# Kernel tuning notes

Hardware: AMD Instinct MI355X
Metric: run time of the kernel (lower is better)

## Reference

```python
import jax, jax.numpy as jnp
import numpy as np

B, S, H, I, E, K = 2, 512, 768, 3072, 8, 1
LB_COEF = 0.01


def _xavier(key, shape, fan_in, fan_out):
    limit = np.sqrt(6.0 / (fan_in + fan_out)).astype(np.float32)
    return jax.random.uniform(key, shape, jnp.float32, -limit, limit)


def setup_inputs() -> dict:
    key = jax.random.key(0)
    k0, k1, k2, k3 = jax.random.split(key, 4)
    return {
        "hidden_states": jax.random.normal(k0, (B, S, H), jnp.float32),
        "gate_w": _xavier(k1, (E, H), H, E),          # nn.Linear(H, E).weight
        "gate_b": jnp.zeros((E,), jnp.float32),
        "w1": _xavier(k2, (E, I, H), H, I),           # per-expert Linear(H, I).weight
        "b1": jnp.zeros((E, I), jnp.float32),
        "w2": _xavier(k3, (E, H, I), I, H),           # per-expert Linear(I, H).weight
        "b2": jnp.zeros((E, H), jnp.float32),
    }


def reference(hidden_states, gate_w, gate_b, w1, b1, w2, b2):
    b, s, h = hidden_states.shape
    x = hidden_states.reshape(-1, h)                      # [T, H]
    gate_logits = x @ gate_w.T + gate_b                   # [T, E]
    top_vals, top_idx = jax.lax.top_k(gate_logits, K)     # [T, K]
    # softmax over the (single) selected logit in fp32 -> all ones, kept for fidelity
    gate_weights = jax.nn.softmax(top_vals.astype(jnp.float32), axis=-1)  # [T, K]

    # load balancing loss (torch.var is unbiased, ddof=1)
    gate_mean = gate_logits.mean(axis=0)                  # [E]
    gate_var = gate_logits.var(axis=0, ddof=1)            # [E]
    lb_loss = LB_COEF * (gate_var / (gate_mean ** 2 + 1e-8)).mean()

    # dense per-expert FFN (exact math; combine picks the routed expert)
    hmid = jnp.einsum('th,eih->tei', x, w1) + b1          # [T, E, I]
    hmid = jax.nn.gelu(hmid, approximate=False)           # torch nn.GELU (erf)
    y = jnp.einsum('tei,ehi->teh', hmid, w2) + b2         # [T, E, H]

    sel = top_idx[:, 0]                                   # [T]
    y_sel = jnp.take_along_axis(y, sel[:, None, None], axis=1)[:, 0]  # [T, H]
    out = y_sel * gate_weights[:, 0:1]                    # weight == 1.0 for k=1
    return out.reshape(b, s, h), lb_loss
```

## Files before the change

kernel.cpp:

```cpp
#include <hip/hip_runtime.h>
#include <hip/hip_bf16.h>
#include <math.h>

#define Hdim 768
#define Idim 3072
#define Tn   1024
#define En   8
#define CAP  256
#define LD2  136

using v4f     = __attribute__((ext_vector_type(4))) float;
using short8  = __attribute__((ext_vector_type(8))) short;
using short4v = __attribute__((ext_vector_type(4))) short;

__device__ inline unsigned short f2bf(float f) {
    unsigned u = __float_as_uint(f);
    u += 0x7fffu + ((u >> 16) & 1u);
    return (unsigned short)(u >> 16);
}
__device__ inline short4v pack4(float4 v) {
    return short4v{ (short)f2bf(v.x), (short)f2bf(v.y), (short)f2bf(v.z), (short)f2bf(v.w) };
}
__device__ __forceinline__ void gl2lds16(const unsigned short* g, unsigned short* l) {
    __builtin_amdgcn_global_load_lds(
        (const __attribute__((address_space(1))) void*)g,
        (__attribute__((address_space(3))) void*)l, 16, 0, 0);
}

__global__ __launch_bounds__(256) void gate_kernel(
    const float* __restrict__ x, const float* __restrict__ gw, const float* __restrict__ gb,
    float* __restrict__ psum, float* __restrict__ psumsq,
    int* __restrict__ sel, int* __restrict__ gcur)
{
    __shared__ float gws[8 * 772];
    __shared__ float lg[8][8];
    int tid = threadIdx.x;
    long t0 = (long)blockIdx.x * 8;
    if (blockIdx.x == 0 && tid < En) gcur[tid] = 0;
    for (int i = tid; i < 8 * 768; i += 256) gws[(i / 768) * 772 + (i % 768)] = gw[i];
    __syncthreads();

    int tok = tid >> 5, e = (tid >> 2) & 7, qr = tid & 3;
    const float4* xp = (const float4*)(x + (t0 + tok) * Hdim) + qr * 48;
    const float4* gp = (const float4*)(gws + e * 772) + qr * 48;
    float a0 = 0.f, a1 = 0.f;
#pragma unroll 8
    for (int i = 0; i < 48; i += 2) {
        float4 xa = xp[i], ga = gp[i], xc = xp[i + 1], gc = gp[i + 1];
        a0 += xa.x * ga.x + xa.y * ga.y + xa.z * ga.z + xa.w * ga.w;
        a1 += xc.x * gc.x + xc.y * gc.y + xc.z * gc.z + xc.w * gc.w;
    }
    float acc = a0 + a1;
    acc += __shfl_xor(acc, 1);
    acc += __shfl_xor(acc, 2);
    if (qr == 0) lg[tok][e] = acc + gb[e];
    __syncthreads();

    if (tid < 8) {
        float best = lg[tid][0]; int bi = 0;
        for (int j = 1; j < 8; j++) { float v = lg[tid][j]; if (v > best) { best = v; bi = j; } }
        sel[t0 + tid] = bi;
    } else if (tid < 16) {
        int e2 = tid - 8;
        float s = 0.f, ss = 0.f;
        for (int t2 = 0; t2 < 8; t2++) { float v = lg[t2][e2]; s += v; ss += v * v; }
        psum[blockIdx.x * 8 + e2]   = s;
        psumsq[blockIdx.x * 8 + e2] = ss;
    }
}

__global__ __launch_bounds__(256) void gather_kernel(
    const float* __restrict__ x, const int* __restrict__ sel,
    const float* __restrict__ psum, const float* __restrict__ psumsq,
    int* __restrict__ gcur, int* __restrict__ perm,
    unsigned short* __restrict__ xb, float* __restrict__ out_lb)
{
    int tid = threadIdx.x;
    if (blockIdx.x == 0 && tid < 64) {
        int e = tid & 7, c0 = (tid >> 3) * 16;
        float s = 0.f, ss = 0.f;
        for (int b = c0; b < c0 + 16; b++) { s += psum[b * 8 + e]; ss += psumsq[b * 8 + e]; }
        s  += __shfl_xor(s, 8);  s  += __shfl_xor(s, 16);  s  += __shfl_xor(s, 32);
        ss += __shfl_xor(ss, 8); ss += __shfl_xor(ss, 16); ss += __shfl_xor(ss, 32);
        if (tid < 8) {
            float mean = s * (1.0f / 1024.0f);
            float var  = (ss - s * mean) * (1.0f / 1023.0f);
            float r = var / (mean * mean + 1e-8f);
            r += __shfl_xor(r, 1); r += __shfl_xor(r, 2); r += __shfl_xor(r, 4);
            if (tid == 0) out_lb[0] = 0.01f * r * 0.125f;
        }
    }
    int t = blockIdx.x * 4 + (tid >> 6);
    int lane = tid & 63;
    int e = sel[t];
    int pos = 0;
    if (lane == 0) pos = atomicAdd(&gcur[e], 1);
    pos = __shfl(pos, 0);
    if (pos < CAP) {
        int slot = (e << 8) + pos;
        if (lane == 0) perm[slot] = t;
        const float4* src = (const float4*)(x + (long)t * Hdim);
        unsigned short* dst = xb + (long)slot * Hdim;
#pragma unroll
        for (int i = 0; i < 3; i++) {
            int c = lane + 64 * i;
            *(short4v*)(dst + c * 4) = pack4(src[c]);
        }
    }
}

__device__ __forceinline__ void gemm_tile_64x64(
    const unsigned short* __restrict__ Arow0, long lda,
    const float* __restrict__ Bn0, long ldb,
    int nloc, int m0, unsigned short* As, unsigned short* Bs, v4f acc[4])
{
    int tid = threadIdx.x;
    int lane = tid & 63, wave = tid >> 6;
    int quad = lane >> 4, l16 = lane & 15;

    const unsigned short* aG[4];
    unsigned short* aL[4];
#pragma unroll
    for (int i = 0; i < 4; i++) {
        int p = (wave * 4 + i) * 64 + lane;
        int row = p >> 4;
        int kc = (p & 15) ^ (row & 15);
        int m = m0 + row; int mm = m < nloc ? m : nloc - 1;
        aG[i] = Arow0 + (long)mm * lda + kc * 8;
        aL[i] = As + p * 8;
    }
    int kq5 = tid & 31, rb8 = tid >> 5;
    const float* bp = Bn0 + (long)rb8 * ldb + kq5 * 4;
    unsigned short* bw = Bs + rb8 * LD2 + kq5 * 4;

    float4 nb[8];
#pragma unroll
    for (int s = 0; s < 8; s++) nb[s] = *(const float4*)(bp + (long)(8 * s) * ldb);

    for (int kb = 0; kb < 768; kb += 128) {
        __syncthreads();
#pragma unroll
        for (int i = 0; i < 4; i++) gl2lds16(aG[i] + kb, aL[i]);
#pragma unroll
        for (int s = 0; s < 8; s++)
            *(short4v*)(bw + s * 8 * LD2) = pack4(nb[s]);
        __syncthreads();
        if (kb + 128 < 768) {
#pragma unroll
            for (int s = 0; s < 8; s++)
                nb[s] = *(const float4*)(bp + (long)(8 * s) * ldb + kb + 128);
        }
#pragma unroll
        for (int s = 0; s < 4; s++) {
            int r = (wave << 4) + l16;
            short8 af = *(const short8*)(As + r * 128 + (((s * 4 + quad) ^ (r & 15)) * 8));
#pragma unroll
            for (int j = 0; j < 4; j++) {
                short8 bf = *(const short8*)(Bs + (j * 16 + l16) * LD2 + s * 32 + quad * 8);
                acc[j] = __builtin_amdgcn_mfma_f32_16x16x32_bf16(af, bf, acc[j], 0, 0, 0);
            }
        }
    }
}

__global__ __launch_bounds__(256) void gemm1_kernel(
    const unsigned short* __restrict__ xb, const float* __restrict__ w1, const float* __restrict__ b1,
    const int* __restrict__ count, unsigned short* __restrict__ hmid)
{
    int e = blockIdx.z;
    int nloc = count[e]; if (nloc > CAP) nloc = CAP;
    int m0 = blockIdx.y << 6;
    if (m0 >= nloc) return;
    int n0 = blockIdx.x << 6;
    int off = e << 8;

    __shared__ __align__(16) unsigned short As[64 * 128];
    __shared__ __align__(16) unsigned short Bs[64 * LD2];

    int tid = threadIdx.x;
    int lane = tid & 63, wave = tid >> 6;
    int quad = lane >> 4, l16 = lane & 15;

    v4f acc[4];
#pragma unroll
    for (int j = 0; j < 4; j++) acc[j] = (v4f){0.f, 0.f, 0.f, 0.f};
    gemm_tile_64x64(xb + (long)off * Hdim, Hdim,
                    w1 + ((long)e * Idim + n0) * Hdim, Hdim,
                    nloc, m0, As, Bs, acc);

    int mr = (wave << 4) + quad * 4;
#pragma unroll
    for (int r = 0; r < 4; r++) {
        int m = m0 + mr + r;
        if (m >= nloc) continue;
        long slot = off + m;
#pragma unroll
        for (int j = 0; j < 4; j++) {
            int n = n0 + j * 16 + l16;
            float v = acc[j][r] + b1[e * Idim + n];
            float g = 0.5f * v * (1.0f + erff(v * 0.70710678118654752f));
            hmid[slot * Idim + n] = f2bf(g);
        }
    }
}

__global__ __launch_bounds__(256) void gemm2_kernel(
    const unsigned short* __restrict__ hmid, const float* __restrict__ w2,
    const int* __restrict__ count, const int* __restrict__ perm,
    float* __restrict__ parts)
{
    int e = blockIdx.z;
    int nloc = count[e]; if (nloc > CAP) nloc = CAP;
    int m0 = blockIdx.y << 6;
    if (m0 >= nloc) return;
    int bx = blockIdx.x;
    int n0 = (bx % 12) << 6;
    int kc4 = bx / 12;
    long kbase = (long)kc4 * 768;
    int off = e << 8;

    __shared__ __align__(16) unsigned short As[64 * 128];
    __shared__ __align__(16) unsigned short Bs[64 * LD2];

    int tid = threadIdx.x;
    int lane = tid & 63, wave = tid >> 6;
    int quad = lane >> 4, l16 = lane & 15;

    v4f acc[4];
#pragma unroll
    for (int j = 0; j < 4; j++) acc[j] = (v4f){0.f, 0.f, 0.f, 0.f};
    gemm_tile_64x64(hmid + (long)off * Idim + kbase, Idim,
                    w2 + ((long)e * Hdim + n0) * Idim + kbase, Idim,
                    nloc, m0, As, Bs, acc);

    float* pout = parts + (long)kc4 * Tn * Hdim;
    int mr = (wave << 4) + quad * 4;
#pragma unroll
    for (int r = 0; r < 4; r++) {
        int m = m0 + mr + r;
        if (m >= nloc) continue;
        int t = perm[off + m];
#pragma unroll
        for (int j = 0; j < 4; j++) {
            int n = n0 + j * 16 + l16;
            pout[(long)t * Hdim + n] = acc[j][r];
        }
    }
}

__global__ __launch_bounds__(256) void reduce_kernel(
    const float* __restrict__ parts, const float* __restrict__ b2,
    const int* __restrict__ sel, float* __restrict__ out)
{
    int idx = blockIdx.x * 256 + threadIdx.x;
    int t = idx / 192, n4 = idx - t * 192;
    int e = sel[t];
    const float4* p = (const float4*)parts;
    float4 a = p[idx];
    float4 b = p[idx + 196608];
    float4 c = p[idx + 393216];
    float4 d = p[idx + 589824];
    float4 bias = ((const float4*)(b2 + (long)e * Hdim))[n4];
    float4 r;
    r.x = a.x + b.x + c.x + d.x + bias.x;
    r.y = a.y + b.y + c.y + d.y + bias.y;
    r.z = a.z + b.z + c.z + d.z + bias.z;
    r.w = a.w + b.w + c.w + d.w + bias.w;
    ((float4*)out)[idx] = r;
}

extern "C" void kernel_launch(void* const* d_in, const int* in_sizes, int n_in,
                              void* d_out, int out_size, void* d_ws, size_t ws_size,
                              hipStream_t stream)
{
    const float* x  = (const float*)d_in[0];
    const float* gw = (const float*)d_in[1];
    const float* gb = (const float*)d_in[2];
    const float* w1 = (const float*)d_in[3];
    const float* b1 = (const float*)d_in[4];
    const float* w2 = (const float*)d_in[5];
    const float* b2 = (const float*)d_in[6];
    float* out = (float*)d_out;

    int*   gcur   = (int*)d_ws;
    int*   sel    = (int*)((char*)d_ws + 128);
    float* psum   = (float*)((char*)d_ws + 4352);
    float* psumsq = (float*)((char*)d_ws + 8448);
    int*   perm   = (int*)((char*)d_ws + 12544);
    unsigned short* xb   = (unsigned short*)((char*)d_ws + 32768);
    unsigned short* hmid = (unsigned short*)((char*)d_ws + (1u << 22));
    float* parts = (float*)((char*)d_ws + (1u << 25));

    gate_kernel  <<<128, 256, 0, stream>>>(x, gw, gb, psum, psumsq, sel, gcur);
    gather_kernel<<<256, 256, 0, stream>>>(x, sel, psum, psumsq, gcur, perm, xb,
                                           out + (long)Tn * Hdim);
    gemm1_kernel <<<dim3(48, 4, 8), 256, 0, stream>>>(xb, w1, b1, gcur, hmid);
    gemm2_kernel <<<dim3(48, 4, 8), 256, 0, stream>>>(hmid, w2, gcur, perm, parts);
    reduce_kernel<<<768, 256, 0, stream>>>(parts, b2, sel, out);
}
```

Baseline: 236.3 us.

## Fuse gate with gather and replace split-K reduce with atomic accumulation

Merges the gating and gather kernels into one: each block computes logits, claims expert slots with atomics, packs its tokens to bf16 and pre-fills the output with the b2 bias. The load-balance loss is moved into gemm1's first block. The four split-K partial buffers and the reduce kernel are removed, with gemm2 atomically adding into the output instead. This cuts two launches and the partials' global traffic, at the cost of a memset launch and float atomics that contend and make the summation order nondeterministic.

```diff
diff --git a/kernel.cpp b/kernel.cpp
--- a/kernel.cpp
+++ b/kernel.cpp
@@ -27,16 +27,19 @@
         (__attribute__((address_space(3))) void*)l, 16, 0, 0);
 }
 
-__global__ __launch_bounds__(256) void gate_kernel(
+__global__ __launch_bounds__(256) void gatecat_kernel(
     const float* __restrict__ x, const float* __restrict__ gw, const float* __restrict__ gb,
+    const float* __restrict__ b2,
     float* __restrict__ psum, float* __restrict__ psumsq,
-    int* __restrict__ sel, int* __restrict__ gcur)
+    int* __restrict__ gcur, int* __restrict__ perm,
+    unsigned short* __restrict__ xb, float* __restrict__ out)
 {
     __shared__ float gws[8 * 772];
     __shared__ float lg[8][8];
+    __shared__ int ssel[8];
+    __shared__ int sslot[8];
     int tid = threadIdx.x;
     long t0 = (long)blockIdx.x * 8;
-    if (blockIdx.x == 0 && tid < En) gcur[tid] = 0;
     for (int i = tid; i < 8 * 768; i += 256) gws[(i / 768) * 772 + (i % 768)] = gw[i];
     __syncthreads();
 
@@ -59,7 +62,8 @@
     if (tid < 8) {
         float best = lg[tid][0]; int bi = 0;
         for (int j = 1; j < 8; j++) { float v = lg[tid][j]; if (v > best) { best = v; bi = j; } }
-        sel[t0 + tid] = bi;
+        ssel[tid] = bi;
+        sslot[tid] = atomicAdd(&gcur[bi], 1);
     } else if (tid < 16) {
         int e2 = tid - 8;
         float s = 0.f, ss = 0.f;
@@ -67,16 +71,94 @@
         psum[blockIdx.x * 8 + e2]   = s;
         psumsq[blockIdx.x * 8 + e2] = ss;
     }
-}
-
-__global__ __launch_bounds__(256) void gather_kernel(
-    const float* __restrict__ x, const int* __restrict__ sel,
+    __syncthreads();
+
+    int lane = tid & 63, wave = tid >> 6;
+#pragma unroll
+    for (int k = 0; k < 2; k++) {
+        int tl = wave * 2 + k;
+        long t = t0 + tl;
+        int e2 = ssel[tl];
+        int pos = sslot[tl];
+        if (pos < CAP) {
+            int slot = (e2 << 8) + pos;
+            if (lane == 0) perm[slot] = (int)t;
+            const float4* src  = (const float4*)(x + t * Hdim);
+            const float4* bsrc = (const float4*)(b2 + (long)e2 * Hdim);
+            unsigned short* dst = xb + (long)slot * Hdim;
+            float4* odst = (float4*)(out + t * Hdim);
+#pragma unroll
+            for (int i = 0; i < 3; i++) {
+                int c = lane + 64 * i;
+                *(short4v*)(dst + c * 4) = pack4(src[c]);
+                odst[c] = bsrc[c];
+            }
+        }
+    }
+}
+
+__device__ __forceinline__ void gemm_tile_64x64(
+    const unsigned short* __restrict__ Arow0, long lda,
+    const float* __restrict__ Bn0, long ldb,
+    int nloc, int m0, unsigned short* As, unsigned short* Bs, v4f acc[4])
+{
+    int tid = threadIdx.x;
+    int lane = tid & 63, wave = tid >> 6;
+    int quad = lane >> 4, l16 = lane & 15;
+
+    const unsigned short* aG[4];
+    unsigned short* aL[4];
+#pragma unroll
+    for (int i = 0; i < 4; i++) {
+        int p = (wave * 4 + i) * 64 + lane;
+        int row = p >> 4;
+        int kc = (p & 15) ^ (row & 15);
+        int m = m0 + row; int mm = m < nloc ? m : nloc - 1;
+        aG[i] = Arow0 + (long)mm * lda + kc * 8;
+        aL[i] = As + p * 8;
+    }
+    int kq5 = tid & 31, rb8 = tid >> 5;
+    const float* bp = Bn0 + (long)rb8 * ldb + kq5 * 4;
+    unsigned short* bw = Bs + rb8 * LD2 + kq5 * 4;
+
+    float4 nb[8];
+#pragma unroll
+    for (int s = 0; s < 8; s++) nb[s] = *(const float4*)(bp + (long)(8 * s) * ldb);
+
+    for (int kb = 0; kb < 768; kb += 128) {
+        __syncthreads();
+#pragma unroll
+        for (int i = 0; i < 4; i++) gl2lds16(aG[i] + kb, aL[i]);
+#pragma unroll
+        for (int s = 0; s < 8; s++)
+            *(short4v*)(bw + s * 8 * LD2) = pack4(nb[s]);
+        __syncthreads();
+        if (kb + 128 < 768) {
+#pragma unroll
+            for (int s = 0; s < 8; s++)
+                nb[s] = *(const float4*)(bp + (long)(8 * s) * ldb + kb + 128);
+        }
+#pragma unroll
+        for (int s = 0; s < 4; s++) {
+            int r = (wave << 4) + l16;
+            short8 af = *(const short8*)(As + r * 128 + (((s * 4 + quad) ^ (r & 15)) * 8));
+#pragma unroll
+            for (int j = 0; j < 4; j++) {
+                short8 bf = *(const short8*)(Bs + (j * 16 + l16) * LD2 + s * 32 + quad * 8);
+                acc[j] = __builtin_amdgcn_mfma_f32_16x16x32_bf16(af, bf, acc[j], 0, 0, 0);
+            }
+        }
+    }
+}
+
+__global__ __launch_bounds__(256) void gemm1_kernel(
+    const unsigned short* __restrict__ xb, const float* __restrict__ w1, const float* __restrict__ b1,
+    const int* __restrict__ count,
     const float* __restrict__ psum, const float* __restrict__ psumsq,
-    int* __restrict__ gcur, int* __restrict__ perm,
-    unsigned short* __restrict__ xb, float* __restrict__ out_lb)
-{
-    int tid = threadIdx.x;
-    if (blockIdx.x == 0 && tid < 64) {
+    unsigned short* __restrict__ hmid, float* __restrict__ out_lb)
+{
+    int tid = threadIdx.x;
+    if (blockIdx.x == 0 && blockIdx.y == 0 && blockIdx.z == 0 && tid < 64) {
         int e = tid & 7, c0 = (tid >> 3) * 16;
         float s = 0.f, ss = 0.f;
         for (int b = c0; b < c0 + 16; b++) { s += psum[b * 8 + e]; ss += psumsq[b * 8 + e]; }
@@ -90,83 +172,7 @@
             if (tid == 0) out_lb[0] = 0.01f * r * 0.125f;
         }
     }
-    int t = blockIdx.x * 4 + (tid >> 6);
-    int lane = tid & 63;
-    int e = sel[t];
-    int pos = 0;
-    if (lane == 0) pos = atomicAdd(&gcur[e], 1);
-    pos = __shfl(pos, 0);
-    if (pos < CAP) {
-        int slot = (e << 8) + pos;
-        if (lane == 0) perm[slot] = t;
-        const float4* src = (const float4*)(x + (long)t * Hdim);
-        unsigned short* dst = xb + (long)slot * Hdim;
-#pragma unroll
-        for (int i = 0; i < 3; i++) {
-            int c = lane + 64 * i;
-            *(short4v*)(dst + c * 4) = pack4(src[c]);
-        }
-    }
-}
-
-__device__ __forceinline__ void gemm_tile_64x64(
-    const unsigned short* __restrict__ Arow0, long lda,
-    const float* __restrict__ Bn0, long ldb,
-    int nloc, int m0, unsigned short* As, unsigned short* Bs, v4f acc[4])
-{
-    int tid = threadIdx.x;
-    int lane = tid & 63, wave = tid >> 6;
-    int quad = lane >> 4, l16 = lane & 15;
-
-    const unsigned short* aG[4];
-    unsigned short* aL[4];
-#pragma unroll
-    for (int i = 0; i < 4; i++) {
-        int p = (wave * 4 + i) * 64 + lane;
-        int row = p >> 4;
-        int kc = (p & 15) ^ (row & 15);
-        int m = m0 + row; int mm = m < nloc ? m : nloc - 1;
-        aG[i] = Arow0 + (long)mm * lda + kc * 8;
-        aL[i] = As + p * 8;
-    }
-    int kq5 = tid & 31, rb8 = tid >> 5;
-    const float* bp = Bn0 + (long)rb8 * ldb + kq5 * 4;
-    unsigned short* bw = Bs + rb8 * LD2 + kq5 * 4;
-
-    float4 nb[8];
-#pragma unroll
-    for (int s = 0; s < 8; s++) nb[s] = *(const float4*)(bp + (long)(8 * s) * ldb);
-
-    for (int kb = 0; kb < 768; kb += 128) {
-        __syncthreads();
-#pragma unroll
-        for (int i = 0; i < 4; i++) gl2lds16(aG[i] + kb, aL[i]);
-#pragma unroll
-        for (int s = 0; s < 8; s++)
-            *(short4v*)(bw + s * 8 * LD2) = pack4(nb[s]);
-        __syncthreads();
-        if (kb + 128 < 768) {
-#pragma unroll
-            for (int s = 0; s < 8; s++)
-                nb[s] = *(const float4*)(bp + (long)(8 * s) * ldb + kb + 128);
-        }
-#pragma unroll
-        for (int s = 0; s < 4; s++) {
-            int r = (wave << 4) + l16;
-            short8 af = *(const short8*)(As + r * 128 + (((s * 4 + quad) ^ (r & 15)) * 8));
-#pragma unroll
-            for (int j = 0; j < 4; j++) {
-                short8 bf = *(const short8*)(Bs + (j * 16 + l16) * LD2 + s * 32 + quad * 8);
-                acc[j] = __builtin_amdgcn_mfma_f32_16x16x32_bf16(af, bf, acc[j], 0, 0, 0);
-            }
-        }
-    }
-}
-
-__global__ __launch_bounds__(256) void gemm1_kernel(
-    const unsigned short* __restrict__ xb, const float* __restrict__ w1, const float* __restrict__ b1,
-    const int* __restrict__ count, unsigned short* __restrict__ hmid)
-{
+
     int e = blockIdx.z;
     int nloc = count[e]; if (nloc > CAP) nloc = CAP;
     int m0 = blockIdx.y << 6;
@@ -177,7 +183,6 @@
     __shared__ __align__(16) unsigned short As[64 * 128];
     __shared__ __align__(16) unsigned short Bs[64 * LD2];
 
-    int tid = threadIdx.x;
     int lane = tid & 63, wave = tid >> 6;
     int quad = lane >> 4, l16 = lane & 15;
 
@@ -207,7 +212,7 @@
 __global__ __launch_bounds__(256) void gemm2_kernel(
     const unsigned short* __restrict__ hmid, const float* __restrict__ w2,
     const int* __restrict__ count, const int* __restrict__ perm,
-    float* __restrict__ parts)
+    float* __restrict__ out)
 {
     int e = blockIdx.z;
     int nloc = count[e]; if (nloc > CAP) nloc = CAP;
@@ -233,7 +238,6 @@
                     w2 + ((long)e * Hdim + n0) * Idim + kbase, Idim,
                     nloc, m0, As, Bs, acc);
 
-    float* pout = parts + (long)kc4 * Tn * Hdim;
     int mr = (wave << 4) + quad * 4;
 #pragma unroll
     for (int r = 0; r < 4; r++) {
@@ -243,30 +247,9 @@
 #pragma unroll
         for (int j = 0; j < 4; j++) {
             int n = n0 + j * 16 + l16;
-            pout[(long)t * Hdim + n] = acc[j][r];
-        }
-    }
-}
-
-__global__ __launch_bounds__(256) void reduce_kernel(
-    const float* __restrict__ parts, const float* __restrict__ b2,
-    const int* __restrict__ sel, float* __restrict__ out)
-{
-    int idx = blockIdx.x * 256 + threadIdx.x;
-    int t = idx / 192, n4 = idx - t * 192;
-    int e = sel[t];
-    const float4* p = (const float4*)parts;
-    float4 a = p[idx];
-    float4 b = p[idx + 196608];
-    float4 c = p[idx + 393216];
-    float4 d = p[idx + 589824];
-    float4 bias = ((const float4*)(b2 + (long)e * Hdim))[n4];
-    float4 r;
-    r.x = a.x + b.x + c.x + d.x + bias.x;
-    r.y = a.y + b.y + c.y + d.y + bias.y;
-    r.z = a.z + b.z + c.z + d.z + bias.z;
-    r.w = a.w + b.w + c.w + d.w + bias.w;
-    ((float4*)out)[idx] = r;
+            atomicAdd(out + (long)t * Hdim + n, acc[j][r]);
+        }
+    }
 }
 
 extern "C" void kernel_launch(void* const* d_in, const int* in_sizes, int n_in,
@@ -283,18 +266,15 @@
     float* out = (float*)d_out;
 
     int*   gcur   = (int*)d_ws;
-    int*   sel    = (int*)((char*)d_ws + 128);
     float* psum   = (float*)((char*)d_ws + 4352);
     float* psumsq = (float*)((char*)d_ws + 8448);
     int*   perm   = (int*)((char*)d_ws + 12544);
     unsigned short* xb   = (unsigned short*)((char*)d_ws + 32768);
     unsigned short* hmid = (unsigned short*)((char*)d_ws + (1u << 22));
-    float* parts = (float*)((char*)d_ws + (1u << 25));
-
-    gate_kernel  <<<128, 256, 0, stream>>>(x, gw, gb, psum, psumsq, sel, gcur);
-    gather_kernel<<<256, 256, 0, stream>>>(x, sel, psum, psumsq, gcur, perm, xb,
-                                           out + (long)Tn * Hdim);
-    gemm1_kernel <<<dim3(48, 4, 8), 256, 0, stream>>>(xb, w1, b1, gcur, hmid);
-    gemm2_kernel <<<dim3(48, 4, 8), 256, 0, stream>>>(hmid, w2, gcur, perm, parts);
-    reduce_kernel<<<768, 256, 0, stream>>>(parts, b2, sel, out);
-}
+
+    hipMemsetAsync(d_ws, 0, 32, stream);
+    gatecat_kernel<<<128, 256, 0, stream>>>(x, gw, gb, b2, psum, psumsq, gcur, perm, xb, out);
+    gemm1_kernel<<<dim3(48, 4, 8), 256, 0, stream>>>(xb, w1, b1, gcur, psum, psumsq, hmid,
+                                                     out + (long)Tn * Hdim);
+    gemm2_kernel<<<dim3(48, 4, 8), 256, 0, stream>>>(hmid, w2, gcur, perm, out);
+}
```

New measurement: 226.9 us. -4.0%, faster.
